# Kernel tuning notes

Measured on AMD Instinct MI355X. Metric: run time of the kernel, lower is better.

The kernel has to match this reference:

```python
import math
import jax, jax.numpy as jnp
import numpy as np

B, T, C = 1, 4096, 2048
H, HKV, D = 16, 4, 128
ROPE_DIM = 128
ROPE_BASE = 500000.0
RMS_EPS = 1e-05
CHUNK = 2048
FFN_H = 8192


def rmsnorm(x, w, eps=RMS_EPS):
    var = jnp.mean(x * x, axis=-1, keepdims=True)
    return x * jax.lax.rsqrt(var + eps) * w


def rope_apply(q, k, rd=ROPE_DIM, base=ROPE_BASE):
    # q, k: [B, H, T, D]; rotate the first rd dims with interleaved pairs.
    b, h, t, d = q.shape
    rd = min(rd, d)
    inv_freq = 1.0 / (base ** (jnp.arange(0, rd, 2, dtype=jnp.float32) / rd))
    pos = jnp.arange(t, dtype=jnp.float32)
    freqs = pos[:, None] * inv_freq[None, :]              # [T, rd//2]
    cos = jnp.cos(freqs)[None, None]                      # [1,1,T,rd//2]
    sin = jnp.sin(freqs)[None, None]

    def _apply(x):
        x1 = x[..., :rd].reshape(b, x.shape[1], t, rd // 2, 2)
        a, bb = x1[..., 0], x1[..., 1]
        a2 = a * cos - bb * sin
        b3 = a * sin + bb * cos
        y1 = jnp.stack([a2, b3], axis=-1).reshape(b, x.shape[1], t, rd)
        return jnp.concatenate([y1, x[..., rd:]], axis=-1)

    return _apply(q), _apply(k)


def chunked_attention(q, k, v, attn_bias, chunk_size=CHUNK):
    # q,k,v: [B,H,T,D]; attn_bias broadcastable to [B,H,T,T].
    b, h, t, d = q.shape
    scale = 1.0 / math.sqrt(d)
    nc = t // chunk_size
    # [nc, B, H, cs, D]
    qc = q.reshape(b, h, nc, chunk_size, d).transpose(2, 0, 1, 3, 4)
    bias = jnp.broadcast_to(attn_bias, attn_bias.shape[:2] + (t, t))
    bc = bias.reshape(bias.shape[0], bias.shape[1], nc, chunk_size, t).transpose(2, 0, 1, 3, 4)

    def one_chunk(args):
        qs, bs = args
        s = jnp.einsum('bhqd,bhkd->bhqk', qs, k) * scale + bs
        p = jax.nn.softmax(s.astype(jnp.float32), axis=-1).astype(q.dtype)
        return jnp.einsum('bhqk,bhkd->bhqd', p, v)

    oc = jax.lax.map(one_chunk, (qc, bc))                 # [nc,B,H,cs,D]
    return oc.transpose(1, 2, 0, 3, 4).reshape(b, h, t, d)


def l4_block(x, attn_bias, attn_norm_w, wq, wk, wv, wo,
             ffn_norm_w, w_gate, w_up, w_down):
    b, t, c = x.shape
    h = rmsnorm(x, attn_norm_w)
    q = (h @ wq.T).reshape(b, t, H, D).transpose(0, 2, 1, 3)    # [B,H,T,D]
    k = (h @ wk.T).reshape(b, t, HKV, D).transpose(0, 2, 1, 3)  # [B,HKV,T,D]
    v = (h @ wv.T).reshape(b, t, HKV, D).transpose(0, 2, 1, 3)
    q, k = rope_apply(q, k)
    rep = H // HKV
    k = jnp.repeat(k, rep, axis=1)                              # GQA expand
    v = jnp.repeat(v, rep, axis=1)
    y = chunked_attention(q, k, v, attn_bias)
    y = y.transpose(0, 2, 1, 3).reshape(b, t, H * D)
    x = x + y @ wo.T
    h2 = rmsnorm(x, ffn_norm_w)
    ffn = (jax.nn.silu(h2 @ w_gate.T) * (h2 @ w_up.T)) @ w_down.T
    return x + ffn


def setup_inputs() -> dict:
    key = jax.random.key(0)
    ks = jax.random.split(key, 9)
    std = 0.02
    x = jax.random.normal(ks[0], (B, T, C), dtype=jnp.float32)
    causal = jnp.triu(jnp.ones((T, T), dtype=bool), k=1)
    attn_bias = jnp.where(causal, jnp.float32(-1e9), jnp.float32(0.0))[None, None]
    return {
        'x': x,
        'attn_bias': attn_bias,
        'attn_norm_w': jnp.ones((C,), jnp.float32),
        'wq': jax.random.normal(ks[1], (H * D, C), jnp.float32) * std,
        'wk': jax.random.normal(ks[2], (HKV * D, C), jnp.float32) * std,
        'wv': jax.random.normal(ks[3], (HKV * D, C), jnp.float32) * std,
        'wo': jax.random.normal(ks[4], (C, H * D), jnp.float32) * std,
        'ffn_norm_w': jnp.ones((C,), jnp.float32),
        'w_gate': jax.random.normal(ks[5], (FFN_H, C), jnp.float32) * std,
        'w_up': jax.random.normal(ks[6], (FFN_H, C), jnp.float32) * std,
        'w_down': jax.random.normal(ks[7], (C, FFN_H), jnp.float32) * std,
    }


def reference(x, attn_bias, attn_norm_w, wq, wk, wv, wo,
              ffn_norm_w, w_gate, w_up, w_down):
    return l4_block(x, attn_bias, attn_norm_w, wq, wk, wv, wo,
                    ffn_norm_w, w_gate, w_up, w_down)
```

## Files before the change

### kernel.cpp

```cpp
#include <hip/hip_runtime.h>
#include <math.h>

#define DEVI static __device__ __forceinline__

typedef __attribute__((ext_vector_type(8))) short bf16x8;
typedef __attribute__((ext_vector_type(4))) short bf16x4;
typedef __attribute__((ext_vector_type(8))) unsigned short ushort8;
typedef __attribute__((ext_vector_type(4))) unsigned short us4;
typedef __attribute__((ext_vector_type(4))) float f32x4;

DEVI unsigned short f32_bf16(float f) {
  unsigned int u = __float_as_uint(f);
  u += 0x7fffu + ((u >> 16) & 1u);
  return (unsigned short)(u >> 16);
}
DEVI float bf16_f32(unsigned short h) {
  return __uint_as_float(((unsigned int)h) << 16);
}

DEVI void async16(void* lds, const void* g) {
  __builtin_amdgcn_global_load_lds(
      (const __attribute__((address_space(1))) void*)g,
      (__attribute__((address_space(3))) void*)lds,
      16, 0, 0);
}

#if __has_builtin(__builtin_amdgcn_mfma_f32_16x16x16bf16_1k)
DEVI f32x4 mfma16(bf16x4 a, bf16x4 b, f32x4 c) {
  return __builtin_amdgcn_mfma_f32_16x16x16bf16_1k(a, b, c, 0, 0, 0);
}
#else
DEVI f32x4 mfma16(bf16x4 a, bf16x4 b, f32x4 c) {
  asm volatile("v_mfma_f32_16x16x16_bf16 %0, %1, %2, %0" : "+v"(c) : "v"(a), "v"(b));
  return c;
}
#endif

__global__ __launch_bounds__(256) void cast_bf16_kernel(
    const float* __restrict__ src, unsigned short* __restrict__ dst, long n8) {
  long i = (long)blockIdx.x * 256 + threadIdx.x;
  if (i >= n8) return;
  const float4 a = *(const float4*)(src + i * 8);
  const float4 b = *(const float4*)(src + i * 8 + 4);
  ushort8 o;
  o[0] = f32_bf16(a.x); o[1] = f32_bf16(a.y); o[2] = f32_bf16(a.z); o[3] = f32_bf16(a.w);
  o[4] = f32_bf16(b.x); o[5] = f32_bf16(b.y); o[6] = f32_bf16(b.z); o[7] = f32_bf16(b.w);
  *(ushort8*)(dst + i * 8) = o;
}

__global__ __launch_bounds__(256) void cast_gu_kernel(
    const float* __restrict__ gate, const float* __restrict__ up,
    unsigned short* __restrict__ dst) {
  long i = (long)blockIdx.x * 256 + threadIdx.x;
  long row = i >> 8;
  long col = (i & 255) * 8;
  const float* src = ((row & 1) ? up : gate) + ((row >> 1) << 11) + col;
  const float4 a = *(const float4*)(src);
  const float4 b = *(const float4*)(src + 4);
  ushort8 o;
  o[0] = f32_bf16(a.x); o[1] = f32_bf16(a.y); o[2] = f32_bf16(a.z); o[3] = f32_bf16(a.w);
  o[4] = f32_bf16(b.x); o[5] = f32_bf16(b.y); o[6] = f32_bf16(b.z); o[7] = f32_bf16(b.w);
  *(ushort8*)(dst + i * 8) = o;
}

__global__ __launch_bounds__(256) void rope_table_kernel(float2* __restrict__ tab) {
  int idx = blockIdx.x * 256 + threadIdx.x;
  int t = idx >> 6, i = idx & 63;
  float inv = __expf(-(float)(2 * i) * (1.0f / 128.0f) * 13.122363377404328f);
  float f = (float)t * inv;
  tab[idx] = make_float2(cosf(f), sinf(f));
}

__global__ __launch_bounds__(256) void rope_apply_kernel(
    unsigned short* __restrict__ qkv, const float2* __restrict__ tab) {
  const int row = blockIdx.x;
  const int tid = threadIdx.x;
#pragma unroll
  for (int it = 0; it < 5; ++it) {
    int p = tid + it * 256;
    int head = p >> 6, i = p & 63;
    int col = (p < 1024) ? (head * 128 + 2 * i) : (2048 + (head - 16) * 128 + 2 * i);
    unsigned short* ptr = qkv + (long)row * 3072 + col;
    float a = bf16_f32(ptr[0]), b = bf16_f32(ptr[1]);
    float2 cs = tab[row * 64 + i];
    float a2 = a * cs.x - b * cs.y;
    float b2 = a * cs.y + b * cs.x;
    ptr[0] = f32_bf16(a2);
    ptr[1] = f32_bf16(b2);
  }
}

__global__ __launch_bounds__(256) void rmsnorm_kernel(
    const float* __restrict__ x, const float* __restrict__ wgt,
    unsigned short* __restrict__ out) {
  __shared__ float red[4];
  const int row = blockIdx.x;
  const int tid = threadIdx.x;
  const float* xr = x + (long)row * 2048 + tid * 8;
  const float4 v0 = *(const float4*)(xr);
  const float4 v1 = *(const float4*)(xr + 4);
  float ss = v0.x * v0.x + v0.y * v0.y + v0.z * v0.z + v0.w * v0.w +
             v1.x * v1.x + v1.y * v1.y + v1.z * v1.z + v1.w * v1.w;
#pragma unroll
  for (int off = 1; off < 64; off <<= 1) ss += __shfl_xor(ss, off);
  if ((tid & 63) == 0) red[tid >> 6] = ss;
  __syncthreads();
  float tot = red[0] + red[1] + red[2] + red[3];
  float sc = rsqrtf(tot * (1.0f / 2048.0f) + 1e-5f);
  const float4 w0 = *(const float4*)(wgt + tid * 8);
  const float4 w1 = *(const float4*)(wgt + tid * 8 + 4);
  ushort8 o;
  o[0] = f32_bf16(v0.x * sc * w0.x); o[1] = f32_bf16(v0.y * sc * w0.y);
  o[2] = f32_bf16(v0.z * sc * w0.z); o[3] = f32_bf16(v0.w * sc * w0.w);
  o[4] = f32_bf16(v1.x * sc * w1.x); o[5] = f32_bf16(v1.y * sc * w1.y);
  o[6] = f32_bf16(v1.z * sc * w1.z); o[7] = f32_bf16(v1.w * sc * w1.w);
  *(ushort8*)(out + (long)row * 2048 + tid * 8) = o;
}

template <int BN, int EPI>
__global__ __launch_bounds__(512, 2) void gemm_p(
    const unsigned short* __restrict__ A, const unsigned short* __restrict__ B,
    void* __restrict__ Cout, const float* __restrict__ res, int M, int N, int K) {
  constexpr int MH = (BN == 256) ? 2 : 1;
  constexpr int MF = MH * 4;
  constexpr int BL = (BN == 256) ? 2 : 1;
  __shared__ __align__(16) unsigned short As[4][256 * 32];
  __shared__ __align__(16) unsigned short Bs[4][BN * 32];

  const int tid = threadIdx.x;
  const int lane = tid & 63;
  const int w = tid >> 6;
  const int c = lane & 15, g = lane >> 4;
  const int wm = (BN == 256) ? (w >> 2) * 128 : (w >> 1) * 64;
  const int wn = (BN == 256) ? (w & 3) * 64 : (w & 1) * 64;

  const int id = blockIdx.y * gridDim.x + blockIdx.x;
  const int cpx = (gridDim.x * gridDim.y) >> 3;
  const int sid = (id & 7) * cpx + (id >> 3);
  const int bx = sid % gridDim.x;
  const int by = sid / gridDim.x;
  const long m0 = (long)bx * 256;
  const long n0 = (long)by * BN;

  const f32x4 fzero = {0.f, 0.f, 0.f, 0.f};
  f32x4 acc[MF][4];
#pragma unroll
  for (int i = 0; i < MF; ++i)
#pragma unroll
    for (int j = 0; j < 4; ++j) acc[i][j] = fzero;

  auto stageA = [&](int buf, int k0) {
#pragma unroll
    for (int q = 0; q < 2; ++q) {
      int G = q * 512 + tid;
      async16(&As[buf][(q * 512 + (tid & ~63)) * 8],
              A + (m0 + (G >> 2)) * (long)K + k0 + (G & 3) * 8);
    }
  };
  auto stageB = [&](int buf, int k0) {
#pragma unroll
    for (int q = 0; q < BL; ++q) {
      int G = q * 512 + tid;
      async16(&Bs[buf][(q * 512 + (tid & ~63)) * 8],
              B + (n0 + (G >> 2)) * (long)K + k0 + (G & 3) * 8);
    }
  };

  const int NT = K >> 5;
  stageA(0, 0);
  stageB(0, 0);
  stageA(1, 32);
  stageB(1, 32);
  if constexpr (BN == 256)
    asm volatile("s_waitcnt vmcnt(4)" ::: "memory");
  else
    asm volatile("s_waitcnt vmcnt(3)" ::: "memory");
  __builtin_amdgcn_s_barrier();

  for (int t = 0; t < NT; ++t) {
    const int buf = t & 3;
    const unsigned short* Ab = As[buf];
    const unsigned short* Bb = Bs[buf];
    const bool pf = (t + 2 < NT);
    const int nb = (t + 2) & 3;

    bf16x8 bfr[4];
#pragma unroll
    for (int nf = 0; nf < 4; ++nf)
      bfr[nf] = *(const bf16x8*)(Bb + (wn + nf * 16 + c) * 32 + g * 8);

#pragma unroll
    for (int mh = 0; mh < MH; ++mh) {
      bf16x8 af[4];
#pragma unroll
      for (int mf = 0; mf < 4; ++mf)
        af[mf] = *(const bf16x8*)(Ab + (wm + mh * 64 + mf * 16 + c) * 32 + g * 8);
      if (pf) {
        if (mh == 0) stageA(nb, (t + 2) << 5);
        if (mh == MH - 1) stageB(nb, (t + 2) << 5);
      }
      __builtin_amdgcn_sched_barrier(0);
      __builtin_amdgcn_s_setprio(1);
#pragma unroll
      for (int mf = 0; mf < 4; ++mf)
#pragma unroll
        for (int nf = 0; nf < 4; ++nf)
          acc[mh * 4 + mf][nf] = __builtin_amdgcn_mfma_f32_16x16x32_bf16(
              af[mf], bfr[nf], acc[mh * 4 + mf][nf], 0, 0, 0);
      __builtin_amdgcn_s_setprio(0);
    }

    if (pf) {
      if constexpr (BN == 256)
        asm volatile("s_waitcnt vmcnt(4)" ::: "memory");
      else
        asm volatile("s_waitcnt vmcnt(3)" ::: "memory");
    } else {
      asm volatile("s_waitcnt vmcnt(0)" ::: "memory");
    }
    __builtin_amdgcn_s_barrier();
  }

#pragma unroll
  for (int i = 0; i < MF; ++i) {
#pragma unroll
    for (int j = 0; j < 4; ++j) {
      const long row0 = m0 + wm + i * 16 + g * 4;
      const long col = n0 + wn + j * 16 + c;
#pragma unroll
      for (int r = 0; r < 4; ++r) {
        float v = acc[i][j][r];
        if (EPI == 0) {
          ((unsigned short*)Cout)[(row0 + r) * N + col] = f32_bf16(v);
        } else if (EPI == 1) {
          ((float*)Cout)[(row0 + r) * N + col] = res[(row0 + r) * N + col] + v;
        } else {
          float other = __shfl_xor(v, 1);
          if (!(c & 1)) {
            float sg = v / (1.0f + __expf(-v));
            ((unsigned short*)Cout)[(row0 + r) * (long)(N >> 1) + (col >> 1)] =
                f32_bf16(sg * other);
          }
        }
      }
    }
  }
}

__global__ __launch_bounds__(256) void transpose_v(
    const unsigned short* __restrict__ qkv, unsigned short* __restrict__ vT) {
  __shared__ __align__(16) unsigned short tile[64][72];
  const int tx = blockIdx.x;
  const int dx = blockIdx.y;
  const int tid = threadIdx.x;
  const int r = tid >> 3, cg = tid & 7;
#pragma unroll
  for (int it = 0; it < 2; ++it) {
    const unsigned short* src =
        qkv + (long)(tx * 64 + r + it * 32) * 3072 + 2560 + dx * 64 + cg * 8;
    *(ushort8*)(&tile[r + it * 32][cg * 8]) = *(const ushort8*)src;
  }
  __syncthreads();
#pragma unroll
  for (int it = 0; it < 2; ++it) {
    int d = r + it * 32;
    ushort8 v;
#pragma unroll
    for (int j = 0; j < 8; ++j) v[j] = tile[cg * 8 + j][d];
    *(ushort8*)(vT + (long)(dx * 64 + d) * 4096 + tx * 64 + cg * 8) = v;
  }
}

__global__ __launch_bounds__(512, 2) void attn_kernel(
    const unsigned short* __restrict__ qkv, const unsigned short* __restrict__ vT,
    unsigned short* __restrict__ y) {
  constexpr float SCL = 0.08838834764831845f * 1.4426950408889634f;
  __shared__ __align__(16) unsigned short Kb[2][64 * 128];
  __shared__ __align__(16) unsigned short Vb[2][128 * 64];

  const int tid = threadIdx.x;
  const int lane = tid & 63;
  const int w = tid >> 6;
  const int c = lane & 15, g = lane >> 4;
  const int h = blockIdx.x >> 4;
  const int pid = blockIdx.x & 15;
  const int kvh = h >> 2;
  const int qt = (w < 4) ? pid : (31 - pid);
  const int q0w = qt * 128 + (w & 3) * 32;
  const int nsteps = 2 * (31 - pid) + 2;

  const f32x4 fzero = {0.f, 0.f, 0.f, 0.f};

  bf16x8 qf[2][4];
#pragma unroll
  for (int mt = 0; mt < 2; ++mt)
#pragma unroll
    for (int kk = 0; kk < 4; ++kk)
      qf[mt][kk] = *(const bf16x8*)(qkv + (long)(q0w + mt * 16 + c) * 3072 +
                                    h * 128 + kk * 32 + g * 8);

  f32x4 o[2][8];
#pragma unroll
  for (int mt = 0; mt < 2; ++mt)
#pragma unroll
    for (int dt = 0; dt < 8; ++dt) o[mt][dt] = fzero;
  float m[2] = {-1e30f, -1e30f}, l[2] = {0.f, 0.f};

  auto stage = [&](int buf, int kv0) {
#pragma unroll
    for (int k = 0; k < 2; ++k) {
      int G = k * 512 + tid;
      int row = G >> 4, colg = (G & 15) ^ (row & 7);
      async16(&Kb[buf][(k * 512 + (tid & ~63)) * 8],
              qkv + (long)(kv0 + row) * 3072 + 2048 + kvh * 128 + colg * 8);
    }
#pragma unroll
    for (int k = 0; k < 2; ++k) {
      int G = k * 512 + tid;
      int row = G >> 3, colg = (G & 7) ^ (row & 7);
      async16(&Vb[buf][(k * 512 + (tid & ~63)) * 8],
              vT + (long)(kvh * 128 + row) * 4096 + kv0 + colg * 8);
    }
  };

  stage(0, 0);
  for (int s = 0; s < nsteps; ++s) {
    const int kv0 = s * 64;
    const int bi = s & 1;
    if (s + 1 < nsteps) {
      stage(bi ^ 1, kv0 + 64);
      asm volatile("s_waitcnt vmcnt(4)" ::: "memory");
    } else {
      asm volatile("s_waitcnt vmcnt(0)" ::: "memory");
    }
    __builtin_amdgcn_s_barrier();
    if (kv0 <= q0w + 31) {
      const unsigned short* Ks = Kb[bi];
      const unsigned short* Vs = Vb[bi];
      f32x4 sv[2][4];
#pragma unroll
      for (int mt = 0; mt < 2; ++mt)
#pragma unroll
        for (int nt = 0; nt < 4; ++nt) sv[mt][nt] = fzero;
#pragma unroll
      for (int kk = 0; kk < 4; ++kk) {
        bf16x8 kf[4];
#pragma unroll
        for (int nt = 0; nt < 4; ++nt)
          kf[nt] = *(const bf16x8*)(Ks + (nt * 16 + c) * 128 +
                                    (((kk * 4 + g) ^ (c & 7)) << 3));
#pragma unroll
        for (int mt = 0; mt < 2; ++mt)
#pragma unroll
          for (int nt = 0; nt < 4; ++nt)
            sv[mt][nt] = __builtin_amdgcn_mfma_f32_16x16x32_bf16(
                kf[nt], qf[mt][kk], sv[mt][nt], 0, 0, 0);
      }
      const bool need_mask = (kv0 + 63 > q0w);
      float al[2];
#pragma unroll
      for (int mt = 0; mt < 2; ++mt) {
        const int qrow = q0w + mt * 16 + c;
#pragma unroll
        for (int nt = 0; nt < 4; ++nt)
#pragma unroll
          for (int r = 0; r < 4; ++r) {
            float xx = sv[mt][nt][r] * SCL;
            if (need_mask && (kv0 + nt * 16 + g * 4 + r > qrow)) xx = -3.0e38f;
            sv[mt][nt][r] = xx;
          }
        float mx = -3.0e38f;
#pragma unroll
        for (int nt = 0; nt < 4; ++nt)
#pragma unroll
          for (int r = 0; r < 4; ++r) mx = fmaxf(mx, sv[mt][nt][r]);
        mx = fmaxf(mx, __shfl_xor(mx, 16));
        mx = fmaxf(mx, __shfl_xor(mx, 32));
        const float mn = fmaxf(m[mt], mx);
        const float a = exp2f(m[mt] - mn);
        m[mt] = mn;
        al[mt] = a;
        float rs = 0.f;
#pragma unroll
        for (int nt = 0; nt < 4; ++nt)
#pragma unroll
          for (int r = 0; r < 4; ++r) {
            float p = exp2f(sv[mt][nt][r] - mn);
            sv[mt][nt][r] = p;
            rs += p;
          }
        rs += __shfl_xor(rs, 16);
        rs += __shfl_xor(rs, 32);
        l[mt] = l[mt] * a + rs;
#pragma unroll
        for (int dt = 0; dt < 8; ++dt) o[mt][dt] *= al[mt];
      }
#pragma unroll
      for (int nt = 0; nt < 4; ++nt) {
        bf16x4 pb[2];
#pragma unroll
        for (int mt = 0; mt < 2; ++mt) {
          int lo_, hi_;
          float s0 = sv[mt][nt][0], s1 = sv[mt][nt][1];
          float s2 = sv[mt][nt][2], s3 = sv[mt][nt][3];
          asm("v_cvt_pk_bf16_f32 %0, %1, %2" : "=v"(lo_) : "v"(s0), "v"(s1));
          asm("v_cvt_pk_bf16_f32 %0, %1, %2" : "=v"(hi_) : "v"(s2), "v"(s3));
          int2 pk = make_int2(lo_, hi_);
          pb[mt] = __builtin_bit_cast(bf16x4, pk);
        }
#pragma unroll
        for (int dt = 0; dt < 8; ++dt) {
          bf16x4 vt = *(const bf16x4*)(Vs + (dt * 16 + c) * 64 +
                                       (((nt * 2 + (g >> 1)) ^ (c & 7)) << 3) +
                                       (g & 1) * 4);
          o[0][dt] = mfma16(vt, pb[0], o[0][dt]);
          o[1][dt] = mfma16(vt, pb[1], o[1][dt]);
        }
      }
    }
    __builtin_amdgcn_s_barrier();
  }
#pragma unroll
  for (int mt = 0; mt < 2; ++mt) {
    const float inv = 1.0f / l[mt];
    const long qrow = q0w + mt * 16 + c;
#pragma unroll
    for (int dt = 0; dt < 8; ++dt) {
      us4 st;
      st[0] = f32_bf16(o[mt][dt][0] * inv);
      st[1] = f32_bf16(o[mt][dt][1] * inv);
      st[2] = f32_bf16(o[mt][dt][2] * inv);
      st[3] = f32_bf16(o[mt][dt][3] * inv);
      *(us4*)(y + qrow * 2048 + h * 128 + dt * 16 + g * 4) = st;
    }
  }
}

extern "C" void kernel_launch(void* const* d_in, const int* in_sizes, int n_in,
                              void* d_out, int out_size, void* d_ws, size_t ws_size,
                              hipStream_t stream) {
  (void)in_sizes; (void)n_in; (void)out_size; (void)ws_size;
  const float* x      = (const float*)d_in[0];
  const float* attn_w = (const float*)d_in[2];
  const float* wq     = (const float*)d_in[3];
  const float* wk     = (const float*)d_in[4];
  const float* wv     = (const float*)d_in[5];
  const float* wo     = (const float*)d_in[6];
  const float* ffn_w  = (const float*)d_in[7];
  const float* wg     = (const float*)d_in[8];
  const float* wu     = (const float*)d_in[9];
  const float* wd     = (const float*)d_in[10];
  float* out = (float*)d_out;

  char* ws = (char*)d_ws;
  size_t off = 0;
  auto alloc = [&](size_t bytes) {
    char* p = ws + off;
    off += (bytes + 255) & ~(size_t)255;
    return p;
  };
  float2* rope_tab        = (float2*)alloc(4096UL * 64 * sizeof(float2));
  unsigned short* wqkv_b  = (unsigned short*)alloc(3072UL * 2048 * 2);
  unsigned short* wo_b    = (unsigned short*)alloc(2048UL * 2048 * 2);
  unsigned short* wgu_b   = (unsigned short*)alloc(16384UL * 2048 * 2);
  unsigned short* wd_b    = (unsigned short*)alloc(2048UL * 8192 * 2);
  unsigned short* h_b     = (unsigned short*)alloc(4096UL * 2048 * 2);
  unsigned short* qkv_b   = (unsigned short*)alloc(4096UL * 3072 * 2);
  unsigned short* vT_b    = (unsigned short*)alloc(512UL * 4096 * 2);
  unsigned short* y_b     = (unsigned short*)alloc(4096UL * 2048 * 2);
  float* r1               = (float*)alloc(4096UL * 2048 * 4);
  unsigned short* t_b     = (unsigned short*)alloc(4096UL * 8192 * 2);

  cast_bf16_kernel<<<2048, 256, 0, stream>>>(wq, wqkv_b, 524288);
  cast_bf16_kernel<<<512, 256, 0, stream>>>(wk, wqkv_b + 2048L * 2048, 131072);
  cast_bf16_kernel<<<512, 256, 0, stream>>>(wv, wqkv_b + 2560L * 2048, 131072);
  cast_bf16_kernel<<<2048, 256, 0, stream>>>(wo, wo_b, 524288);
  cast_gu_kernel<<<16384, 256, 0, stream>>>(wg, wu, wgu_b);
  cast_bf16_kernel<<<8192, 256, 0, stream>>>(wd, wd_b, 2097152);
  rope_table_kernel<<<1024, 256, 0, stream>>>(rope_tab);

  rmsnorm_kernel<<<4096, 256, 0, stream>>>(x, attn_w, h_b);
  {
    dim3 grid(16, 12);
    gemm_p<256, 0><<<grid, 512, 0, stream>>>(h_b, wqkv_b, qkv_b, nullptr, 4096, 3072, 2048);
  }
  rope_apply_kernel<<<4096, 256, 0, stream>>>(qkv_b, rope_tab);
  {
    dim3 grid(64, 8);
    transpose_v<<<grid, 256, 0, stream>>>(qkv_b, vT_b);
  }
  attn_kernel<<<256, 512, 0, stream>>>(qkv_b, vT_b, y_b);
  {
    dim3 grid(16, 16);
    gemm_p<128, 1><<<grid, 512, 0, stream>>>(y_b, wo_b, r1, x, 4096, 2048, 2048);
  }

  rmsnorm_kernel<<<4096, 256, 0, stream>>>(r1, ffn_w, h_b);
  {
    dim3 grid(16, 64);
    gemm_p<256, 2><<<grid, 512, 0, stream>>>(h_b, wgu_b, t_b, nullptr, 4096, 16384, 2048);
  }
  {
    dim3 grid(16, 16);
    gemm_p<128, 1><<<grid, 512, 0, stream>>>(t_b, wd_b, out, r1, 4096, 2048, 8192);
  }
}
```

Measured before the change: 899.7 us.

## Restructure GEMM into 8-wave ping-pong with BK=64 and XOR-swizzled LDS

Rewrites the shared GEMM kernel to use a K-step of 64 with two LDS buffers instead of four buffers of K=32. Each tile is split into halves, and the loads are issued in four phases, each separated by barriers, so global loads interleave with MFMA work. A row-dependent XOR swizzle on the 16-byte chunks is meant to avoid LDS bank conflicts on the wider rows. The extra barriers per K-step and the hand-tuned vmcnt counts add sync overhead and risk, in exchange for fewer loop iterations and conflict-free fragment reads.

After: 950.8 us, median of 4. 1.06x slower.

```diff
diff --git a/kernel.cpp b/kernel.cpp
--- a/kernel.cpp
+++ b/kernel.cpp
@@ -118,21 +118,24 @@
 }
 
 template <int BN, int EPI>
-__global__ __launch_bounds__(512, 2) void gemm_p(
+__global__ __launch_bounds__(512, 2) void gemm8p(
     const unsigned short* __restrict__ A, const unsigned short* __restrict__ B,
     void* __restrict__ Cout, const float* __restrict__ res, int M, int N, int K) {
-  constexpr int MH = (BN == 256) ? 2 : 1;
-  constexpr int MF = MH * 4;
+  constexpr int MQ = (BN == 256) ? 4 : 2;
+  constexpr int AL = 2;
   constexpr int BL = (BN == 256) ? 2 : 1;
-  __shared__ __align__(16) unsigned short As[4][256 * 32];
-  __shared__ __align__(16) unsigned short Bs[4][BN * 32];
+  constexpr int HB = (BN / 2) * 64;
+  __shared__ __align__(16) unsigned short As[2][256 * 64];
+  __shared__ __align__(16) unsigned short Bs[2][BN * 64];
 
   const int tid = threadIdx.x;
   const int lane = tid & 63;
   const int w = tid >> 6;
   const int c = lane & 15, g = lane >> 4;
-  const int wm = (BN == 256) ? (w >> 2) * 128 : (w >> 1) * 64;
-  const int wn = (BN == 256) ? (w & 3) * 64 : (w & 1) * 64;
+  const int a_grp = (BN == 256) ? (w >> 2) : (w >> 1);
+  const int b_grp = (BN == 256) ? (w & 3) : (w & 1);
+  const int sw0 = ((g ^ (c & 7)) << 3);
+  const int sw1 = (((4 + g) ^ (c & 7)) << 3);
 
   const int id = blockIdx.y * gridDim.x + blockIdx.x;
   const int cpx = (gridDim.x * gridDim.y) >> 3;
@@ -143,103 +146,136 @@
   const long n0 = (long)by * BN;
 
   const f32x4 fzero = {0.f, 0.f, 0.f, 0.f};
-  f32x4 acc[MF][4];
-#pragma unroll
-  for (int i = 0; i < MF; ++i)
-#pragma unroll
-    for (int j = 0; j < 4; ++j) acc[i][j] = fzero;
-
-  auto stageA = [&](int buf, int k0) {
-#pragma unroll
-    for (int q = 0; q < 2; ++q) {
+  f32x4 acc[2][MQ][2][2];
+#pragma unroll
+  for (int qm = 0; qm < 2; ++qm)
+#pragma unroll
+    for (int mf = 0; mf < MQ; ++mf)
+#pragma unroll
+      for (int qn = 0; qn < 2; ++qn)
+#pragma unroll
+        for (int nf = 0; nf < 2; ++nf) acc[qm][mf][qn][nf] = fzero;
+
+  auto stageA = [&](int buf, int h, int k0) {
+#pragma unroll
+    for (int q = 0; q < AL; ++q) {
       int G = q * 512 + tid;
-      async16(&As[buf][(q * 512 + (tid & ~63)) * 8],
-              A + (m0 + (G >> 2)) * (long)K + k0 + (G & 3) * 8);
+      int ks = (G & 7) ^ ((G >> 3) & 7);
+      async16(&As[buf][h * 8192 + (q * 512 + (tid & ~63)) * 8],
+              A + (m0 + h * 128 + (G >> 3)) * (long)K + k0 + ks * 8);
     }
   };
-  auto stageB = [&](int buf, int k0) {
+  auto stageB = [&](int buf, int h, int k0) {
 #pragma unroll
     for (int q = 0; q < BL; ++q) {
       int G = q * 512 + tid;
-      async16(&Bs[buf][(q * 512 + (tid & ~63)) * 8],
-              B + (n0 + (G >> 2)) * (long)K + k0 + (G & 3) * 8);
+      int ks = (G & 7) ^ ((G >> 3) & 7);
+      async16(&Bs[buf][h * HB + (q * 512 + (tid & ~63)) * 8],
+              B + (n0 + h * (BN / 2) + (G >> 3)) * (long)K + k0 + ks * 8);
     }
   };
 
-  const int NT = K >> 5;
-  stageA(0, 0);
-  stageB(0, 0);
-  stageA(1, 32);
-  stageB(1, 32);
+  const int NT = K >> 6;
+  stageA(0, 0, 0);
+  stageB(0, 0, 0);
+  stageB(0, 1, 0);
+  stageA(0, 1, 0);
   if constexpr (BN == 256)
     asm volatile("s_waitcnt vmcnt(4)" ::: "memory");
   else
     asm volatile("s_waitcnt vmcnt(3)" ::: "memory");
   __builtin_amdgcn_s_barrier();
 
+  bf16x8 af[MQ][2];
+  bf16x8 bfr[2][2][2];
+
   for (int t = 0; t < NT; ++t) {
-    const int buf = t & 3;
+    const int buf = t & 1;
     const unsigned short* Ab = As[buf];
     const unsigned short* Bb = Bs[buf];
-    const bool pf = (t + 2 < NT);
-    const int nb = (t + 2) & 3;
-
-    bf16x8 bfr[4];
-#pragma unroll
-    for (int nf = 0; nf < 4; ++nf)
-      bfr[nf] = *(const bf16x8*)(Bb + (wn + nf * 16 + c) * 32 + g * 8);
-
-#pragma unroll
-    for (int mh = 0; mh < MH; ++mh) {
-      bf16x8 af[4];
-#pragma unroll
-      for (int mf = 0; mf < 4; ++mf)
-        af[mf] = *(const bf16x8*)(Ab + (wm + mh * 64 + mf * 16 + c) * 32 + g * 8);
+    const bool pf = (t + 1 < NT);
+    const int nbuf = buf ^ 1;
+    const int k1 = (t + 1) << 6;
+
+#pragma unroll
+    for (int ph = 0; ph < 4; ++ph) {
+      const int qm = ph >> 1, qn = ph & 1;
+      if (ph == 0 || ph == 2) {
+#pragma unroll
+        for (int mf = 0; mf < MQ; ++mf) {
+          const int row = a_grp * (MQ * 16) + mf * 16 + c;
+          af[mf][0] = *(const bf16x8*)(Ab + qm * 8192 + row * 64 + sw0);
+          af[mf][1] = *(const bf16x8*)(Ab + qm * 8192 + row * 64 + sw1);
+        }
+      }
+      if (ph == 0 || ph == 1) {
+#pragma unroll
+        for (int nf = 0; nf < 2; ++nf) {
+          const int row = b_grp * 32 + nf * 16 + c;
+          bfr[ph][nf][0] = *(const bf16x8*)(Bb + ph * HB + row * 64 + sw0);
+          bfr[ph][nf][1] = *(const bf16x8*)(Bb + ph * HB + row * 64 + sw1);
+        }
+      }
       if (pf) {
-        if (mh == 0) stageA(nb, (t + 2) << 5);
-        if (mh == MH - 1) stageB(nb, (t + 2) << 5);
-      }
+        if (ph == 0) stageA(nbuf, 0, k1);
+        if (ph == 1) stageB(nbuf, 0, k1);
+        if (ph == 2) stageB(nbuf, 1, k1);
+        if (ph == 3) stageA(nbuf, 1, k1);
+      }
+      __builtin_amdgcn_s_barrier();
+      asm volatile("s_waitcnt lgkmcnt(0)" ::: "memory");
       __builtin_amdgcn_sched_barrier(0);
       __builtin_amdgcn_s_setprio(1);
 #pragma unroll
-      for (int mf = 0; mf < 4; ++mf)
-#pragma unroll
-        for (int nf = 0; nf < 4; ++nf)
-          acc[mh * 4 + mf][nf] = __builtin_amdgcn_mfma_f32_16x16x32_bf16(
-              af[mf], bfr[nf], acc[mh * 4 + mf][nf], 0, 0, 0);
+      for (int kk = 0; kk < 2; ++kk)
+#pragma unroll
+        for (int mf = 0; mf < MQ; ++mf)
+#pragma unroll
+          for (int nf = 0; nf < 2; ++nf)
+            acc[qm][mf][qn][nf] = __builtin_amdgcn_mfma_f32_16x16x32_bf16(
+                af[mf][kk], bfr[qn][nf][kk], acc[qm][mf][qn][nf], 0, 0, 0);
       __builtin_amdgcn_s_setprio(0);
-    }
-
-    if (pf) {
-      if constexpr (BN == 256)
-        asm volatile("s_waitcnt vmcnt(4)" ::: "memory");
-      else
-        asm volatile("s_waitcnt vmcnt(3)" ::: "memory");
-    } else {
-      asm volatile("s_waitcnt vmcnt(0)" ::: "memory");
-    }
-    __builtin_amdgcn_s_barrier();
-  }
-
-#pragma unroll
-  for (int i = 0; i < MF; ++i) {
-#pragma unroll
-    for (int j = 0; j < 4; ++j) {
-      const long row0 = m0 + wm + i * 16 + g * 4;
-      const long col = n0 + wn + j * 16 + c;
-#pragma unroll
-      for (int r = 0; r < 4; ++r) {
-        float v = acc[i][j][r];
-        if (EPI == 0) {
-          ((unsigned short*)Cout)[(row0 + r) * N + col] = f32_bf16(v);
-        } else if (EPI == 1) {
-          ((float*)Cout)[(row0 + r) * N + col] = res[(row0 + r) * N + col] + v;
-        } else {
-          float other = __shfl_xor(v, 1);
-          if (!(c & 1)) {
-            float sg = v / (1.0f + __expf(-v));
-            ((unsigned short*)Cout)[(row0 + r) * (long)(N >> 1) + (col >> 1)] =
-                f32_bf16(sg * other);
+      if (pf) {
+        if (ph == 0) asm volatile("s_waitcnt vmcnt(4)" ::: "memory");
+        if (ph == 1 || ph == 3) {
+          if constexpr (BN == 256)
+            asm volatile("s_waitcnt vmcnt(4)" ::: "memory");
+          else
+            asm volatile("s_waitcnt vmcnt(3)" ::: "memory");
+        }
+      } else {
+        if (ph == 0) asm volatile("s_waitcnt vmcnt(2)" ::: "memory");
+        if (ph == 1) asm volatile("s_waitcnt vmcnt(0)" ::: "memory");
+      }
+      __builtin_amdgcn_s_barrier();
+    }
+  }
+
+#pragma unroll
+  for (int qm = 0; qm < 2; ++qm) {
+#pragma unroll
+    for (int mf = 0; mf < MQ; ++mf) {
+#pragma unroll
+      for (int qn = 0; qn < 2; ++qn) {
+#pragma unroll
+        for (int nf = 0; nf < 2; ++nf) {
+          const long row0 = m0 + qm * 128 + a_grp * (MQ * 16) + mf * 16 + g * 4;
+          const long col = n0 + qn * (BN / 2) + b_grp * 32 + nf * 16 + c;
+#pragma unroll
+          for (int r = 0; r < 4; ++r) {
+            float v = acc[qm][mf][qn][nf][r];
+            if (EPI == 0) {
+              ((unsigned short*)Cout)[(row0 + r) * N + col] = f32_bf16(v);
+            } else if (EPI == 1) {
+              ((float*)Cout)[(row0 + r) * N + col] = res[(row0 + r) * N + col] + v;
+            } else {
+              float other = __shfl_xor(v, 1);
+              if (!(c & 1)) {
+                float sg = v / (1.0f + __expf(-v));
+                ((unsigned short*)Cout)[(row0 + r) * (long)(N >> 1) + (col >> 1)] =
+                    f32_bf16(sg * other);
+              }
+            }
           }
         }
       }
@@ -482,7 +518,7 @@
   rmsnorm_kernel<<<4096, 256, 0, stream>>>(x, attn_w, h_b);
   {
     dim3 grid(16, 12);
-    gemm_p<256, 0><<<grid, 512, 0, stream>>>(h_b, wqkv_b, qkv_b, nullptr, 4096, 3072, 2048);
+    gemm8p<256, 0><<<grid, 512, 0, stream>>>(h_b, wqkv_b, qkv_b, nullptr, 4096, 3072, 2048);
   }
   rope_apply_kernel<<<4096, 256, 0, stream>>>(qkv_b, rope_tab);
   {
@@ -492,16 +528,16 @@
   attn_kernel<<<256, 512, 0, stream>>>(qkv_b, vT_b, y_b);
   {
     dim3 grid(16, 16);
-    gemm_p<128, 1><<<grid, 512, 0, stream>>>(y_b, wo_b, r1, x, 4096, 2048, 2048);
+    gemm8p<128, 1><<<grid, 512, 0, stream>>>(y_b, wo_b, r1, x, 4096, 2048, 2048);
   }
 
   rmsnorm_kernel<<<4096, 256, 0, stream>>>(r1, ffn_w, h_b);
   {
     dim3 grid(16, 64);
-    gemm_p<256, 2><<<grid, 512, 0, stream>>>(h_b, wgu_b, t_b, nullptr, 4096, 16384, 2048);
+    gemm8p<256, 2><<<grid, 512, 0, stream>>>(h_b, wgu_b, t_b, nullptr, 4096, 16384, 2048);
   }
   {
     dim3 grid(16, 16);
-    gemm_p<128, 1><<<grid, 512, 0, stream>>>(t_b, wd_b, out, r1, 4096, 2048, 8192);
-  }
-}
+    gemm8p<128, 1><<<grid, 512, 0, stream>>>(t_b, wd_b, out, r1, 4096, 2048, 8192);
+  }
+}
```
